# Performance work log

Measured on AMD Instinct MI355X. Metric: run time of the kernel, lower is better.

Reference implementation:

```python
import jax, jax.numpy as jnp
import numpy as np

N_NODES = 50000
N_EDGES = 600000
D = 128
HIDDEN = 128
N_GRAPHS = 128
N_CLASSES = 10
N_STACKED = 3  # num_layers - 1


def setup_inputs() -> dict:
    key = jax.random.key(0)
    ks = jax.random.split(key, 12)
    s = 1.0 / np.sqrt(HIDDEN)
    inp = {
        "x": jax.random.normal(ks[0], (N_NODES, D), dtype=jnp.float32),
        "edge_index": jax.random.randint(ks[1], (2, N_EDGES), 0, N_NODES, dtype=jnp.int64),
        "batch": jnp.sort(jax.random.randint(ks[2], (N_NODES,), 0, N_GRAPHS, dtype=jnp.int64)),
        "W1": jax.random.normal(ks[3], (D, HIDDEN), dtype=jnp.float32) * s,
        "R1": jax.random.normal(ks[4], (D, HIDDEN), dtype=jnp.float32) * s,
        "b1": jnp.zeros((HIDDEN,), dtype=jnp.float32),
        "Wc": jax.random.normal(ks[5], (N_STACKED, HIDDEN, HIDDEN), dtype=jnp.float32) * s,
        "Rc": jax.random.normal(ks[6], (N_STACKED, HIDDEN, HIDDEN), dtype=jnp.float32) * s,
        "bc": jnp.zeros((N_STACKED, HIDDEN), dtype=jnp.float32),
        "lin1_w": jax.random.normal(ks[7], (HIDDEN, HIDDEN), dtype=jnp.float32) * s,
        "lin1_b": jnp.zeros((HIDDEN,), dtype=jnp.float32),
        "lin2_w": jax.random.normal(ks[8], (HIDDEN, N_CLASSES), dtype=jnp.float32) * s,
        "lin2_b": jnp.zeros((N_CLASSES,), dtype=jnp.float32),
    }
    return inp


def _gcn_norm(edge_index, n_nodes):
    # symmetric GCN normalization coeffs per edge (edge_weight=None -> ones)
    src, dst = edge_index[0], edge_index[1]
    ones = jnp.ones((edge_index.shape[1],), dtype=jnp.float32)
    deg = jax.ops.segment_sum(ones, dst, num_segments=n_nodes)
    dinv = jnp.where(deg > 0, jax.lax.rsqrt(jnp.maximum(deg, 1.0)), 0.0)
    return dinv[src] * dinv[dst]


def _gcs(x, src, dst, norm, W, R, b):
    # GCN aggregation on transformed features + linear skip (root) connection
    h = x @ W                                   # [N, H]
    msg = h[src] * norm[:, None]                # gather + scale, [E, H]
    agg = jax.ops.segment_sum(msg, dst, num_segments=x.shape[0])
    return agg + x @ R + b


def reference(x, edge_index, batch, W1, R1, b1, Wc, Rc, bc,
              lin1_w, lin1_b, lin2_w, lin2_b):
    src, dst = edge_index[0], edge_index[1]
    norm = _gcn_norm(edge_index, x.shape[0])

    h = jax.nn.relu(_gcs(x, src, dst, norm, W1, R1, b1))
    for i in range(N_STACKED):
        h = jax.nn.relu(_gcs(h, src, dst, norm, Wc[i], Rc[i], bc[i]))
    last = h

    # global mean pool over graphs
    sums = jax.ops.segment_sum(h, batch, num_segments=N_GRAPHS)
    cnts = jax.ops.segment_sum(jnp.ones((h.shape[0],), h.dtype), batch,
                               num_segments=N_GRAPHS)
    pooled = sums / jnp.maximum(cnts, 1.0)[:, None]

    g = jax.nn.relu(pooled @ lin1_w + lin1_b)   # dropout is identity in eval mode
    logits = g @ lin2_w + lin2_b
    return jax.nn.log_softmax(logits, axis=-1), last
```

## Files before the change

kernel.cpp:

```cpp
#include <hip/hip_runtime.h>

#define N_NODES  50000
#define N_EDGES  600000
#define DIM      128
#define N_GRAPHS 128
#define N_CLASSES 10
#define NB_SCAN  196
#define LDSW     136


typedef __bf16 bf16x8 __attribute__((ext_vector_type(8)));
typedef float  f32x4  __attribute__((ext_vector_type(4)));

__device__ inline unsigned short f2bf(float f) {
  union { float f; unsigned int i; } u; u.f = f;
  unsigned int r = u.i + 0x7fff + ((u.i >> 16) & 1);
  return (unsigned short)(r >> 16);
}
__device__ inline float bf2f(unsigned short s) {
  union { unsigned int i; float f; } u; u.i = ((unsigned int)s) << 16;
  return u.f;
}


__global__ __launch_bounds__(256) void k_zero(float* __restrict__ p, int n) {
  int i = blockIdx.x * 256 + threadIdx.x;
  if (i < n) p[i] = 0.f;
}


__global__ __launch_bounds__(256) void k_pack(const float* __restrict__ W1,
                                              const float* __restrict__ R1,
                                              const float* __restrict__ Wc,
                                              const float* __restrict__ Rc,
                                              unsigned short* __restrict__ pk) {
  int mm = blockIdx.y;
  const float* src = (mm == 0) ? W1
                   : (mm < 4)  ? Wc + (size_t)(mm - 1) * DIM * DIM
                   : (mm == 4) ? R1
                               : Rc + (size_t)(mm - 5) * DIM * DIM;
  int idx = blockIdx.x * 256 + threadIdx.x;
  int lane = idx & 63;
  int kc   = (idx >> 6) & 3;
  int nt   = idx >> 8;
  int col  = nt * 16 + (lane & 15);
  int k0   = kc * 32 + (lane >> 4) * 8;
  unsigned short* dst = pk + (size_t)mm * 16384 + (size_t)idx * 8;
  ushort4 u;
  u.x = f2bf(src[(k0 + 0) * DIM + col]);
  u.y = f2bf(src[(k0 + 1) * DIM + col]);
  u.z = f2bf(src[(k0 + 2) * DIM + col]);
  u.w = f2bf(src[(k0 + 3) * DIM + col]);
  *(ushort4*)&dst[0] = u;
  u.x = f2bf(src[(k0 + 4) * DIM + col]);
  u.y = f2bf(src[(k0 + 5) * DIM + col]);
  u.z = f2bf(src[(k0 + 6) * DIM + col]);
  u.w = f2bf(src[(k0 + 7) * DIM + col]);
  *(ushort4*)&dst[4] = u;
}


__global__ __launch_bounds__(256) void k_deg(const int* __restrict__ ei,
                                             int* __restrict__ deg) {
  int e = blockIdx.x * 256 + threadIdx.x;
  if (e < N_EDGES) atomicAdd(&deg[ei[N_EDGES + e]], 1);
}

__global__ __launch_bounds__(256) void k_dinv(const int* __restrict__ deg,
                                              float* __restrict__ dinv) {
  int n = blockIdx.x * 256 + threadIdx.x;
  if (n < N_NODES) {
    int d = deg[n];
    dinv[n] = (d > 0) ? rsqrtf((float)d) : 0.f;
  }
}


__global__ __launch_bounds__(256) void k_bsum(const int* __restrict__ deg,
                                              int* __restrict__ bsum) {
  int i = blockIdx.x * 256 + threadIdx.x;
  int v = (i < N_NODES) ? deg[i] : 0;
  __shared__ int tmp[256];
  int t = threadIdx.x;
  tmp[t] = v;
  __syncthreads();
  for (int off = 128; off > 0; off >>= 1) {
    if (t < off) tmp[t] += tmp[t + off];
    __syncthreads();
  }
  if (t == 0) bsum[blockIdx.x] = tmp[0];
}

__global__ __launch_bounds__(256) void k_bscan(const int* __restrict__ bsum,
                                               int* __restrict__ boff,
                                               int* __restrict__ rowp) {
  int t = threadIdx.x;
  int v = (t < NB_SCAN) ? bsum[t] : 0;
  __shared__ int tmp[256];
  tmp[t] = v;
  __syncthreads();
  for (int off = 1; off < 256; off <<= 1) {
    int add = (t >= off) ? tmp[t - off] : 0;
    __syncthreads();
    tmp[t] += add;
    __syncthreads();
  }
  boff[t] = tmp[t] - v;
  if (t == 0) rowp[N_NODES] = N_EDGES;
}

__global__ __launch_bounds__(256) void k_rowp(const int* __restrict__ deg,
                                              const int* __restrict__ boff,
                                              int* __restrict__ rowp) {
  int i = blockIdx.x * 256 + threadIdx.x;
  int t = threadIdx.x;
  int v = (i < N_NODES) ? deg[i] : 0;
  __shared__ int tmp[256];
  tmp[t] = v;
  __syncthreads();
  for (int off = 1; off < 256; off <<= 1) {
    int add = (t >= off) ? tmp[t - off] : 0;
    __syncthreads();
    tmp[t] += add;
    __syncthreads();
  }
  if (i < N_NODES) rowp[i] = boff[blockIdx.x] + tmp[t] - v;
}

__global__ __launch_bounds__(256) void k_fill(const int* __restrict__ ei,
                                              const int* __restrict__ rowp,
                                              int* __restrict__ cnt,
                                              const float* __restrict__ dinv,
                                              int* __restrict__ csrc,
                                              float* __restrict__ enorm) {
  int e = blockIdx.x * 256 + threadIdx.x;
  if (e < N_EDGES) {
    int s = ei[e];
    int d = ei[N_EDGES + e];
    int p = rowp[d] + atomicAdd(&cnt[d], 1);
    csrc[p] = s;
    enorm[p] = dinv[s] * dinv[d];
  }
}


__global__ __launch_bounds__(256) void k_gemm(const float* __restrict__ xin,
                                              const unsigned short* __restrict__ pkW,
                                              const unsigned short* __restrict__ pkR,
                                              const float* __restrict__ bv,
                                              unsigned short* __restrict__ hwb,
                                              float* __restrict__ xout) {
  __shared__ unsigned short xs[64 * LDSW];
  const int tid = threadIdx.x;
  const int row0 = blockIdx.x * 64;
#pragma unroll
  for (int i = 0; i < 8; ++i) {
    int idx = i * 256 + tid;
    int r = idx >> 5, c4 = (idx & 31) * 4;
    int row = row0 + r;
    float4 v = make_float4(0.f, 0.f, 0.f, 0.f);
    if (row < N_NODES) v = *(const float4*)&xin[row * DIM + c4];
    ushort4 u;
    u.x = f2bf(v.x); u.y = f2bf(v.y); u.z = f2bf(v.z); u.w = f2bf(v.w);
    *(ushort4*)&xs[r * LDSW + c4] = u;
  }
  __syncthreads();

  const int wave = tid >> 6;
  const int lane = tid & 63;
  const int m = lane & 15, q = lane >> 4;

  bf16x8 a[4];
#pragma unroll
  for (int kc = 0; kc < 4; ++kc)
    a[kc] = *(const bf16x8*)&xs[(wave * 16 + m) * LDSW + kc * 32 + q * 8];

  f32x4 acc[16];
#pragma unroll
  for (int t = 0; t < 16; ++t) acc[t] = (f32x4){0.f, 0.f, 0.f, 0.f};

#pragma unroll
  for (int nt = 0; nt < 8; ++nt) {
    const unsigned short* pw = pkW + ((size_t)(nt * 4) * 64 + lane) * 8;
    const unsigned short* pr = pkR + ((size_t)(nt * 4) * 64 + lane) * 8;
#pragma unroll
    for (int kc = 0; kc < 4; ++kc) {
      bf16x8 bW = *(const bf16x8*)(pw + (size_t)kc * 64 * 8);
      acc[nt] = __builtin_amdgcn_mfma_f32_16x16x32_bf16(a[kc], bW, acc[nt], 0, 0, 0);
    }
#pragma unroll
    for (int kc = 0; kc < 4; ++kc) {
      bf16x8 bR = *(const bf16x8*)(pr + (size_t)kc * 64 * 8);
      acc[8 + nt] = __builtin_amdgcn_mfma_f32_16x16x32_bf16(a[kc], bR, acc[8 + nt], 0, 0, 0);
    }
  }

#pragma unroll
  for (int nt = 0; nt < 8; ++nt) {
    int col = nt * 16 + m;
#pragma unroll
    for (int rg = 0; rg < 4; ++rg) {
      int row = row0 + wave * 16 + q * 4 + rg;
      if (row < N_NODES) hwb[row * DIM + col] = f2bf(acc[nt][rg]);
    }
  }
#pragma unroll
  for (int nt = 0; nt < 8; ++nt) {
    int col = nt * 16 + m;
    float bias = bv[col];
#pragma unroll
    for (int rg = 0; rg < 4; ++rg) {
      int row = row0 + wave * 16 + q * 4 + rg;
      if (row < N_NODES) xout[row * DIM + col] = acc[8 + nt][rg] + bias;
    }
  }
}


__global__ __launch_bounds__(256) void k_agg(const unsigned short* __restrict__ hwb,
                                             const int* __restrict__ rowp,
                                             const int* __restrict__ csrc,
                                             const float* __restrict__ enorm,
                                             float* __restrict__ xout) {
  int n = blockIdx.x * 8 + (threadIdx.x >> 5);
  if (n >= N_NODES) return;
  int l4 = (threadIdx.x & 31) * 4;
  float4 acc = *(const float4*)&xout[n * DIM + l4];
  int e = rowp[n], e1 = rowp[n + 1];
  for (; e + 2 <= e1; e += 2) {
    int s0 = csrc[e],  s1 = csrc[e + 1];
    float w0 = enorm[e], w1 = enorm[e + 1];
    ushort4 u0 = *(const ushort4*)&hwb[s0 * DIM + l4];
    ushort4 u1 = *(const ushort4*)&hwb[s1 * DIM + l4];
    acc.x = fmaf(w0, bf2f(u0.x), fmaf(w1, bf2f(u1.x), acc.x));
    acc.y = fmaf(w0, bf2f(u0.y), fmaf(w1, bf2f(u1.y), acc.y));
    acc.z = fmaf(w0, bf2f(u0.z), fmaf(w1, bf2f(u1.z), acc.z));
    acc.w = fmaf(w0, bf2f(u0.w), fmaf(w1, bf2f(u1.w), acc.w));
  }
  if (e < e1) {
    int s0 = csrc[e];
    float w0 = enorm[e];
    ushort4 u0 = *(const ushort4*)&hwb[s0 * DIM + l4];
    acc.x = fmaf(w0, bf2f(u0.x), acc.x);
    acc.y = fmaf(w0, bf2f(u0.y), acc.y);
    acc.z = fmaf(w0, bf2f(u0.z), acc.z);
    acc.w = fmaf(w0, bf2f(u0.w), acc.w);
  }
  acc.x = fmaxf(acc.x, 0.f);
  acc.y = fmaxf(acc.y, 0.f);
  acc.z = fmaxf(acc.z, 0.f);
  acc.w = fmaxf(acc.w, 0.f);
  *(float4*)&xout[n * DIM + l4] = acc;
}


__global__ __launch_bounds__(1024) void k_pool2(const float* __restrict__ h,
                                                const int* __restrict__ batch,
                                                float* __restrict__ pooled) {
  int g = blockIdx.x;
  int t = threadIdx.x;
  __shared__ int sb[2];
  if (t < 2) {
    int target = g + t;
    int lo = 0, hi = N_NODES;
    while (lo < hi) {
      int mid = (lo + hi) >> 1;
      if (batch[mid] < target) lo = mid + 1; else hi = mid;
    }
    sb[t] = lo;
  }
  __syncthreads();
  int start = sb[0], end = sb[1];
  int c = t & 127, rg = t >> 7;
  float acc = 0.f;
  for (int r = start + rg; r < end; r += 8) acc += h[r * DIM + c];
  __shared__ float sp[8][DIM];
  sp[rg][c] = acc;
  __syncthreads();
  if (rg == 0) {
    float tot = acc;
#pragma unroll
    for (int i = 1; i < 8; ++i) tot += sp[i][c];
    float cnt = fmaxf((float)(end - start), 1.f);
    pooled[g * DIM + c] = tot / cnt;
  }
}


__global__ __launch_bounds__(128) void k_mlp1(const float* __restrict__ pooled,
                                              const float* __restrict__ w,
                                              const float* __restrict__ bias,
                                              float* __restrict__ g1) {
  int g = blockIdx.x, t = threadIdx.x;
  __shared__ float sp[DIM];
  sp[t] = pooled[g * DIM + t];
  __syncthreads();
  float acc = bias[t];
#pragma unroll 4
  for (int k = 0; k < DIM; ++k) acc = fmaf(sp[k], w[k * DIM + t], acc);
  g1[g * DIM + t] = fmaxf(acc, 0.f);
}

__global__ __launch_bounds__(128) void k_mlp2(const float* __restrict__ g1,
                                              const float* __restrict__ w,
                                              const float* __restrict__ bias,
                                              float* __restrict__ out) {
  int g = threadIdx.x;
  float l[N_CLASSES];
#pragma unroll
  for (int c = 0; c < N_CLASSES; ++c) l[c] = bias[c];
  for (int k = 0; k < DIM; ++k) {
    float gv = g1[g * DIM + k];
#pragma unroll
    for (int c = 0; c < N_CLASSES; ++c) l[c] = fmaf(gv, w[k * N_CLASSES + c], l[c]);
  }
  float m = l[0];
#pragma unroll
  for (int c = 1; c < N_CLASSES; ++c) m = fmaxf(m, l[c]);
  float s = 0.f;
#pragma unroll
  for (int c = 0; c < N_CLASSES; ++c) s += expf(l[c] - m);
  float lse = logf(s) + m;
#pragma unroll
  for (int c = 0; c < N_CLASSES; ++c) out[g * N_CLASSES + c] = l[c] - lse;
}


extern "C" void kernel_launch(void* const* d_in, const int* in_sizes, int n_in,
                              void* d_out, int out_size, void* d_ws, size_t ws_size,
                              hipStream_t stream) {
  const float* x     = (const float*)d_in[0];
  const int* ei      = (const int*)d_in[1];
  const int* batch   = (const int*)d_in[2];
  const float* W1  = (const float*)d_in[3];
  const float* R1  = (const float*)d_in[4];
  const float* b1  = (const float*)d_in[5];
  const float* Wc  = (const float*)d_in[6];
  const float* Rc  = (const float*)d_in[7];
  const float* bc  = (const float*)d_in[8];
  const float* l1w = (const float*)d_in[9];
  const float* l1b = (const float*)d_in[10];
  const float* l2w = (const float*)d_in[11];
  const float* l2b = (const float*)d_in[12];

  float* out   = (float*)d_out;
  float* dlast = out + N_GRAPHS * N_CLASSES;

  float* ws    = (float*)d_ws;
  unsigned short* hwb = (unsigned short*)ws;
  int*   deg   = (int*)(ws + 3200000);
  int*   cnt   = (int*)(ws + 3250000);
  float* pooled= ws + 3300000;
  float* dinv  = ws + 3316384;
  int*   rowp  = (int*)(ws + 3366384);
  int*   csrc  = (int*)(ws + 3416400);
  float* enorm = ws + 4016400;
  float* g1    = ws + 4616400;
  unsigned short* pk = (unsigned short*)(ws + 4632784);
  int*   bsum  = (int*)(ws + 4698320);
  int*   boff  = (int*)(ws + 4698576);

  k_zero<<<(100000 + 255) / 256, 256, 0, stream>>>(ws + 3200000, 100000);

  k_pack<<<dim3(8, 8), 256, 0, stream>>>(W1, R1, Wc, Rc, pk);
  k_deg <<<(N_EDGES + 255) / 256, 256, 0, stream>>>(ei, deg);
  k_dinv<<<(N_NODES + 255) / 256, 256, 0, stream>>>(deg, dinv);
  k_bsum<<<NB_SCAN, 256, 0, stream>>>(deg, bsum);
  k_bscan<<<1, 256, 0, stream>>>(bsum, boff, rowp);
  k_rowp<<<NB_SCAN, 256, 0, stream>>>(deg, boff, rowp);
  k_fill<<<(N_EDGES + 255) / 256, 256, 0, stream>>>(ei, rowp, cnt, dinv, csrc, enorm);

  const float* xin = x;
  for (int l = 0; l < 4; ++l) {
    const unsigned short* pkW = pk + (size_t)l * 16384;
    const unsigned short* pkR = pk + (size_t)(4 + l) * 16384;
    const float* B = (l == 0) ? b1 : bc + (size_t)(l - 1) * DIM;
    k_gemm<<<(N_NODES + 63) / 64, 256, 0, stream>>>(xin, pkW, pkR, B, hwb, dlast);
    k_agg <<<(N_NODES + 7) / 8, 256, 0, stream>>>(hwb, rowp, csrc, enorm, dlast);
    xin = dlast;
  }

  k_pool2<<<N_GRAPHS, 1024, 0, stream>>>(dlast, batch, pooled);
  k_mlp1<<<N_GRAPHS, 128, 0, stream>>>(pooled, l1w, l1b, g1);
  k_mlp2<<<1, N_GRAPHS, 0, stream>>>(g1, l2w, l2b, out);
}
```

Before: 423.0 us.

## Store intermediate layer activations in bf16 and load GEMM fragments directly

Intermediate activations for the first three layers are now kept in a separate bf16 buffer instead of fp32; only the final layer writes fp32 into the output. This roughly halves activation read and write traffic in both the GEMM and the aggregation kernels. The GEMM also drops its LDS staging and syncthreads, loading MFMA A-fragments straight from global memory. The aggregation loop is unrolled to four edges per iteration for more memory-level parallelism. The cost is extra rounding of the skip and activation values to bf16, which may reduce accuracy, and a templated kernel set.

```diff
diff --git a/kernel.cpp b/kernel.cpp
--- a/kernel.cpp
+++ b/kernel.cpp
@@ -6,7 +6,6 @@
 #define N_GRAPHS 128
 #define N_CLASSES 10
 #define NB_SCAN  196
-#define LDSW     136
 
 
 typedef __bf16 bf16x8 __attribute__((ext_vector_type(8)));
@@ -20,6 +19,17 @@
 __device__ inline float bf2f(unsigned short s) {
   union { unsigned int i; float f; } u; u.i = ((unsigned int)s) << 16;
   return u.f;
+}
+__device__ inline bf16x8 zero8() {
+  union { bf16x8 v; unsigned long long q[2]; } u;
+  u.q[0] = 0ull; u.q[1] = 0ull;
+  return u.v;
+}
+__device__ inline bf16x8 pack8(float4 lo, float4 hi) {
+  union { bf16x8 v; unsigned short s[8]; } u;
+  u.s[0] = f2bf(lo.x); u.s[1] = f2bf(lo.y); u.s[2] = f2bf(lo.z); u.s[3] = f2bf(lo.w);
+  u.s[4] = f2bf(hi.x); u.s[5] = f2bf(hi.y); u.s[6] = f2bf(hi.z); u.s[7] = f2bf(hi.w);
+  return u.v;
 }
 
 
@@ -75,7 +85,6 @@
   }
 }
 
-
 __global__ __launch_bounds__(256) void k_bsum(const int* __restrict__ deg,
                                               int* __restrict__ bsum) {
   int i = blockIdx.x * 256 + threadIdx.x;
@@ -144,36 +153,43 @@
 }
 
 
-__global__ __launch_bounds__(256) void k_gemm(const float* __restrict__ xin,
+template<bool AF32, bool LAST>
+__global__ __launch_bounds__(256) void k_gemm(const void* __restrict__ act,
                                               const unsigned short* __restrict__ pkW,
                                               const unsigned short* __restrict__ pkR,
                                               const float* __restrict__ bv,
                                               unsigned short* __restrict__ hwb,
-                                              float* __restrict__ xout) {
-  __shared__ unsigned short xs[64 * LDSW];
-  const int tid = threadIdx.x;
-  const int row0 = blockIdx.x * 64;
-#pragma unroll
-  for (int i = 0; i < 8; ++i) {
-    int idx = i * 256 + tid;
-    int r = idx >> 5, c4 = (idx & 31) * 4;
-    int row = row0 + r;
-    float4 v = make_float4(0.f, 0.f, 0.f, 0.f);
-    if (row < N_NODES) v = *(const float4*)&xin[row * DIM + c4];
-    ushort4 u;
-    u.x = f2bf(v.x); u.y = f2bf(v.y); u.z = f2bf(v.z); u.w = f2bf(v.w);
-    *(ushort4*)&xs[r * LDSW + c4] = u;
-  }
-  __syncthreads();
-
-  const int wave = tid >> 6;
-  const int lane = tid & 63;
+                                              unsigned short* __restrict__ skipb,
+                                              float* __restrict__ skipf) {
+  const int tid  = threadIdx.x;
+  const int wave = tid >> 6, lane = tid & 63;
   const int m = lane & 15, q = lane >> 4;
+  const int rbase = blockIdx.x * 64 + wave * 16;
+  const int arow  = rbase + m;
+  const bool aok  = arow < N_NODES;
 
   bf16x8 a[4];
-#pragma unroll
-  for (int kc = 0; kc < 4; ++kc)
-    a[kc] = *(const bf16x8*)&xs[(wave * 16 + m) * LDSW + kc * 32 + q * 8];
+  if (AF32) {
+    const float* xf = (const float*)act;
+#pragma unroll
+    for (int kc = 0; kc < 4; ++kc) {
+      float4 lo = make_float4(0.f, 0.f, 0.f, 0.f);
+      float4 hi = make_float4(0.f, 0.f, 0.f, 0.f);
+      if (aok) {
+        lo = *(const float4*)&xf[arow * DIM + kc * 32 + q * 8];
+        hi = *(const float4*)&xf[arow * DIM + kc * 32 + q * 8 + 4];
+      }
+      a[kc] = pack8(lo, hi);
+    }
+  } else {
+    const unsigned short* xb = (const unsigned short*)act;
+#pragma unroll
+    for (int kc = 0; kc < 4; ++kc) {
+      bf16x8 v = zero8();
+      if (aok) v = *(const bf16x8*)&xb[arow * DIM + kc * 32 + q * 8];
+      a[kc] = v;
+    }
+  }
 
   f32x4 acc[16];
 #pragma unroll
@@ -200,7 +216,7 @@
     int col = nt * 16 + m;
 #pragma unroll
     for (int rg = 0; rg < 4; ++rg) {
-      int row = row0 + wave * 16 + q * 4 + rg;
+      int row = rbase + q * 4 + rg;
       if (row < N_NODES) hwb[row * DIM + col] = f2bf(acc[nt][rg]);
     }
   }
@@ -210,34 +226,48 @@
     float bias = bv[col];
 #pragma unroll
     for (int rg = 0; rg < 4; ++rg) {
-      int row = row0 + wave * 16 + q * 4 + rg;
-      if (row < N_NODES) xout[row * DIM + col] = acc[8 + nt][rg] + bias;
-    }
-  }
-}
-
-
+      int row = rbase + q * 4 + rg;
+      if (row < N_NODES) {
+        float v = acc[8 + nt][rg] + bias;
+        if (LAST) skipf[row * DIM + col] = v;
+        else      skipb[row * DIM + col] = f2bf(v);
+      }
+    }
+  }
+}
+
+
+template<bool LAST>
 __global__ __launch_bounds__(256) void k_agg(const unsigned short* __restrict__ hwb,
                                              const int* __restrict__ rowp,
                                              const int* __restrict__ csrc,
                                              const float* __restrict__ enorm,
-                                             float* __restrict__ xout) {
+                                             unsigned short* __restrict__ actb,
+                                             float* __restrict__ actf) {
   int n = blockIdx.x * 8 + (threadIdx.x >> 5);
   if (n >= N_NODES) return;
   int l4 = (threadIdx.x & 31) * 4;
-  float4 acc = *(const float4*)&xout[n * DIM + l4];
+  float4 acc;
+  if (LAST) {
+    acc = *(const float4*)&actf[n * DIM + l4];
+  } else {
+    ushort4 s = *(const ushort4*)&actb[n * DIM + l4];
+    acc = make_float4(bf2f(s.x), bf2f(s.y), bf2f(s.z), bf2f(s.w));
+  }
   int e = rowp[n], e1 = rowp[n + 1];
-  for (; e + 2 <= e1; e += 2) {
-    int s0 = csrc[e],  s1 = csrc[e + 1];
-    float w0 = enorm[e], w1 = enorm[e + 1];
+  for (; e + 4 <= e1; e += 4) {
+    int s0 = csrc[e],     s1 = csrc[e + 1], s2 = csrc[e + 2], s3 = csrc[e + 3];
+    float w0 = enorm[e],  w1 = enorm[e + 1], w2 = enorm[e + 2], w3 = enorm[e + 3];
     ushort4 u0 = *(const ushort4*)&hwb[s0 * DIM + l4];
     ushort4 u1 = *(const ushort4*)&hwb[s1 * DIM + l4];
-    acc.x = fmaf(w0, bf2f(u0.x), fmaf(w1, bf2f(u1.x), acc.x));
-    acc.y = fmaf(w0, bf2f(u0.y), fmaf(w1, bf2f(u1.y), acc.y));
-    acc.z = fmaf(w0, bf2f(u0.z), fmaf(w1, bf2f(u1.z), acc.z));
-    acc.w = fmaf(w0, bf2f(u0.w), fmaf(w1, bf2f(u1.w), acc.w));
-  }
-  if (e < e1) {
+    ushort4 u2 = *(const ushort4*)&hwb[s2 * DIM + l4];
+    ushort4 u3 = *(const ushort4*)&hwb[s3 * DIM + l4];
+    acc.x = fmaf(w0, bf2f(u0.x), fmaf(w1, bf2f(u1.x), fmaf(w2, bf2f(u2.x), fmaf(w3, bf2f(u3.x), acc.x))));
+    acc.y = fmaf(w0, bf2f(u0.y), fmaf(w1, bf2f(u1.y), fmaf(w2, bf2f(u2.y), fmaf(w3, bf2f(u3.y), acc.y))));
+    acc.z = fmaf(w0, bf2f(u0.z), fmaf(w1, bf2f(u1.z), fmaf(w2, bf2f(u2.z), fmaf(w3, bf2f(u3.z), acc.z))));
+    acc.w = fmaf(w0, bf2f(u0.w), fmaf(w1, bf2f(u1.w), fmaf(w2, bf2f(u2.w), fmaf(w3, bf2f(u3.w), acc.w))));
+  }
+  for (; e < e1; ++e) {
     int s0 = csrc[e];
     float w0 = enorm[e];
     ushort4 u0 = *(const ushort4*)&hwb[s0 * DIM + l4];
@@ -250,7 +280,13 @@
   acc.y = fmaxf(acc.y, 0.f);
   acc.z = fmaxf(acc.z, 0.f);
   acc.w = fmaxf(acc.w, 0.f);
-  *(float4*)&xout[n * DIM + l4] = acc;
+  if (LAST) {
+    *(float4*)&actf[n * DIM + l4] = acc;
+  } else {
+    ushort4 o;
+    o.x = f2bf(acc.x); o.y = f2bf(acc.y); o.z = f2bf(acc.z); o.w = f2bf(acc.w);
+    *(ushort4*)&actb[n * DIM + l4] = o;
+  }
 }
 
 
@@ -347,20 +383,21 @@
   float* dlast = out + N_GRAPHS * N_CLASSES;
 
   float* ws    = (float*)d_ws;
-  unsigned short* hwb = (unsigned short*)ws;
-  int*   deg   = (int*)(ws + 3200000);
-  int*   cnt   = (int*)(ws + 3250000);
-  float* pooled= ws + 3300000;
-  float* dinv  = ws + 3316384;
-  int*   rowp  = (int*)(ws + 3366384);
-  int*   csrc  = (int*)(ws + 3416400);
-  float* enorm = ws + 4016400;
-  float* g1    = ws + 4616400;
-  unsigned short* pk = (unsigned short*)(ws + 4632784);
-  int*   bsum  = (int*)(ws + 4698320);
-  int*   boff  = (int*)(ws + 4698576);
-
-  k_zero<<<(100000 + 255) / 256, 256, 0, stream>>>(ws + 3200000, 100000);
+  unsigned short* hwb  = (unsigned short*)ws;
+  unsigned short* actb = (unsigned short*)(ws + 3200000);
+  int*   deg   = (int*)(ws + 6400000);
+  int*   cnt   = (int*)(ws + 6450000);
+  float* pooled= ws + 6500000;
+  float* dinv  = ws + 6516384;
+  int*   rowp  = (int*)(ws + 6566384);
+  int*   csrc  = (int*)(ws + 6616400);
+  float* enorm = ws + 7216400;
+  float* g1    = ws + 7816400;
+  unsigned short* pk = (unsigned short*)(ws + 7832784);
+  int*   bsum  = (int*)(ws + 7898320);
+  int*   boff  = (int*)(ws + 7898576);
+
+  k_zero<<<(100000 + 255) / 256, 256, 0, stream>>>(ws + 6400000, 100000);
 
   k_pack<<<dim3(8, 8), 256, 0, stream>>>(W1, R1, Wc, Rc, pk);
   k_deg <<<(N_EDGES + 255) / 256, 256, 0, stream>>>(ei, deg);
@@ -370,15 +407,23 @@
   k_rowp<<<NB_SCAN, 256, 0, stream>>>(deg, boff, rowp);
   k_fill<<<(N_EDGES + 255) / 256, 256, 0, stream>>>(ei, rowp, cnt, dinv, csrc, enorm);
 
-  const float* xin = x;
-  for (int l = 0; l < 4; ++l) {
-    const unsigned short* pkW = pk + (size_t)l * 16384;
-    const unsigned short* pkR = pk + (size_t)(4 + l) * 16384;
-    const float* B = (l == 0) ? b1 : bc + (size_t)(l - 1) * DIM;
-    k_gemm<<<(N_NODES + 63) / 64, 256, 0, stream>>>(xin, pkW, pkR, B, hwb, dlast);
-    k_agg <<<(N_NODES + 7) / 8, 256, 0, stream>>>(hwb, rowp, csrc, enorm, dlast);
-    xin = dlast;
-  }
+  const int NGB = (N_NODES + 63) / 64;
+  const int NAB = (N_NODES + 7) / 8;
+
+  k_gemm<true, false><<<NGB, 256, 0, stream>>>(
+      x, pk + 0 * 16384, pk + 4 * 16384, b1, hwb, actb, nullptr);
+  k_agg<false><<<NAB, 256, 0, stream>>>(hwb, rowp, csrc, enorm, actb, nullptr);
+
+  for (int l = 1; l <= 2; ++l) {
+    k_gemm<false, false><<<NGB, 256, 0, stream>>>(
+        actb, pk + (size_t)l * 16384, pk + (size_t)(4 + l) * 16384,
+        bc + (size_t)(l - 1) * DIM, hwb, actb, nullptr);
+    k_agg<false><<<NAB, 256, 0, stream>>>(hwb, rowp, csrc, enorm, actb, nullptr);
+  }
+
+  k_gemm<false, true><<<NGB, 256, 0, stream>>>(
+      actb, pk + 3 * 16384, pk + 7 * 16384, bc + 2 * DIM, hwb, nullptr, dlast);
+  k_agg<true><<<NAB, 256, 0, stream>>>(hwb, rowp, csrc, enorm, nullptr, dlast);
 
   k_pool2<<<N_GRAPHS, 1024, 0, stream>>>(dlast, batch, pooled);
   k_mlp1<<<N_GRAPHS, 128, 0, stream>>>(pooled, l1w, l1b, g1);
```

Measured after the change: 402.8 us. 1.05x faster.
